# Optimization experiments

Hardware: AMD Instinct MI355X
Metric: run time of the kernel (lower is better)

The kernel has to match this reference:

```python
import jax, jax.numpy as jnp
import numpy as np

EMB = 1024
HEAD = 128

def setup_inputs() -> dict:
    key = jax.random.key(0)
    kx, kk, kq, kv = jax.random.split(key, 4)
    s = 1.0 / np.sqrt(EMB)
    return {
        "x": jax.random.normal(kx, (8, 2048, EMB), dtype=jnp.float32),
        "Wk": jax.random.normal(kk, (EMB, HEAD), dtype=jnp.float32) * s,
        "Wq": jax.random.normal(kq, (EMB, HEAD), dtype=jnp.float32) * s,
        "Wv": jax.random.normal(kv, (EMB, HEAD), dtype=jnp.float32) * s,
    }

def reference(x, Wk, Wq, Wv):
    # x: [B,T,E]; projections (no bias)
    k = jnp.einsum('bte,eh->bth', x, Wk)
    q = jnp.einsum('bte,eh->bth', x, Wq)
    v = jnp.einsum('bte,eh->bth', x, Wv)
    # scores: [B,T,T], NOTE: no 1/sqrt(d) scaling in original module
    qk = jnp.einsum('bih,bjh->bij', q, k)
    T = x.shape[1]
    causal = jnp.tril(jnp.ones((T, T), dtype=bool))  # True = keep
    qk = jnp.where(causal, qk, -jnp.inf)
    # NOTE: softmax over axis -2 (query axis), as in original
    attn = jax.nn.softmax(qk, axis=-2)
    return jnp.einsum('bij,bjh->bih', attn, v)
```

## Files before the change

kernel.cpp:

```cpp
#include <hip/hip_runtime.h>

typedef unsigned short u16;
typedef unsigned int u32;
typedef _Float16 f16;
typedef __attribute__((ext_vector_type(8))) _Float16 f16x8;
typedef __attribute__((ext_vector_type(4))) float f32x4;

constexpr int SEQ = 2048;
constexpr int EMBD = 1024;
constexpr int HD = 128;
constexpr int NB = 8;
constexpr int NSLS = 8;
constexpr int NSLP = 4;

__device__ inline u16 f2h(float f) { return __builtin_bit_cast(u16, (f16)f); }
__device__ inline u32 pack2(float a, float b) { return (u32)f2h(a) | ((u32)f2h(b) << 16); }

__device__ inline f32x4 mfma16(f16x8 a, f16x8 b, f32x4 c) {
  return __builtin_amdgcn_mfma_f32_16x16x32_f16(a, b, c, 0, 0, 0);
}

__device__ __forceinline__ void gload16(const u16* g, u16* l) {
  __builtin_amdgcn_global_load_lds(
      (const __attribute__((address_space(1))) u32*)g,
      (__attribute__((address_space(3))) u32*)l, 16, 0, 0);
}

template<int RB>
__device__ inline f16x8 frag_ld(const u16* lds, int row, int e) {
  int byte = row * RB + ((e * 2) ^ ((row & 7) << 4));
  return *reinterpret_cast<const f16x8*>(reinterpret_cast<const char*>(lds) + byte);
}

__global__ __launch_bounds__(256) void k_cvt_w(const float* __restrict__ Wq,
                                               const float* __restrict__ Wk,
                                               const float* __restrict__ Wv,
                                               u16* __restrict__ Wt) {
  int t = blockIdx.x * 256 + threadIdx.x;
  int e0 = (t & 255) * 4;
  int H = t >> 8;
  int w = H >> 7, h = H & 127;
  const float* W = (w == 0) ? Wq : (w == 1) ? Wk : Wv;
  ushort4 o;
  o.x = f2h(W[(size_t)(e0 + 0) * HD + h]);
  o.y = f2h(W[(size_t)(e0 + 1) * HD + h]);
  o.z = f2h(W[(size_t)(e0 + 2) * HD + h]);
  o.w = f2h(W[(size_t)(e0 + 3) * HD + h]);
  int k0t = e0 >> 6, ec = e0 & 63;
  size_t el = (size_t)(k0t * 384 + H) * 64 + (ec ^ ((H & 7) << 3));
  *reinterpret_cast<ushort4*>(Wt + el) = o;
}

__global__ __launch_bounds__(512, 4) void k_proj(const float* __restrict__ x,
                                                 const u16* __restrict__ Wt,
                                                 u16* __restrict__ Qb,
                                                 u16* __restrict__ Kb,
                                                 u16* __restrict__ Vtb) {
  __shared__ __align__(16) u16 As[2][64 * 64];
  __shared__ __align__(16) u16 Bs[2][192 * 64];
  const int mt = blockIdx.x, ny = blockIdx.y;
  const int t = threadIdx.x, lane = t & 63, wave = t >> 6;
  const int rh = (wave & 1) * 32, cq = (wave >> 1) * 48;
  const int ar = t >> 3, ac = t & 7;
  const float* asrc = x + (size_t)(mt * 64 + ar) * EMBD + ac * 8;
  const int adst = ar * 64 + ((ac * 8) ^ ((ar & 7) << 3));
  f32x4 zero = {0.f, 0.f, 0.f, 0.f};
  f32x4 acc[2][3];
#pragma unroll
  for (int a = 0; a < 2; ++a)
#pragma unroll
    for (int b = 0; b < 3; ++b) acc[a][b] = zero;

  float4 xe0, xe1, xo0, xo1;
  xe0 = *reinterpret_cast<const float4*>(asrc);
  xe1 = *reinterpret_cast<const float4*>(asrc + 4);
#pragma unroll
  for (int q = 0; q < 3; ++q) {
    int lin = q * 512 + t;
    gload16(Wt + ny * 12288 + lin * 8, &Bs[0][lin * 8]);
  }
  {
    uint4 o = {pack2(xe0.x, xe0.y), pack2(xe0.z, xe0.w), pack2(xe1.x, xe1.y), pack2(xe1.z, xe1.w)};
    *reinterpret_cast<uint4*>(&As[0][adst]) = o;
  }
  xo0 = *reinterpret_cast<const float4*>(asrc + 64);
  xo1 = *reinterpret_cast<const float4*>(asrc + 68);
  __syncthreads();
#pragma unroll 2
  for (int s = 0; s < 16; ++s) {
    const int cur = s & 1;
    if (s + 1 < 16) {
#pragma unroll
      for (int q = 0; q < 3; ++q) {
        int lin = q * 512 + t;
        gload16(Wt + (s + 1) * 24576 + ny * 12288 + lin * 8, &Bs[cur ^ 1][lin * 8]);
      }
    }
    if (s + 2 < 16) {
      if (cur == 0) {
        xe0 = *reinterpret_cast<const float4*>(asrc + (s + 2) * 64);
        xe1 = *reinterpret_cast<const float4*>(asrc + (s + 2) * 64 + 4);
      } else {
        xo0 = *reinterpret_cast<const float4*>(asrc + (s + 2) * 64);
        xo1 = *reinterpret_cast<const float4*>(asrc + (s + 2) * 64 + 4);
      }
    }
    __builtin_amdgcn_s_setprio(1);
#pragma unroll
    for (int kk = 0; kk < 2; ++kk) {
      f16x8 af0 = frag_ld<128>(As[cur], rh + (lane & 15), kk * 32 + (lane >> 4) * 8);
      f16x8 af1 = frag_ld<128>(As[cur], rh + 16 + (lane & 15), kk * 32 + (lane >> 4) * 8);
#pragma unroll
      for (int fc = 0; fc < 3; ++fc) {
        f16x8 bw = frag_ld<128>(Bs[cur], cq + fc * 16 + (lane & 15), kk * 32 + (lane >> 4) * 8);
        acc[0][fc] = mfma16(af0, bw, acc[0][fc]);
        acc[1][fc] = mfma16(af1, bw, acc[1][fc]);
      }
    }
    __builtin_amdgcn_s_setprio(0);
    if (s + 1 < 16) {
      uint4 o;
      if (cur == 0)
        o = {pack2(xo0.x, xo0.y), pack2(xo0.z, xo0.w), pack2(xo1.x, xo1.y), pack2(xo1.z, xo1.w)};
      else
        o = {pack2(xe0.x, xe0.y), pack2(xe0.z, xe0.w), pack2(xe1.x, xe1.y), pack2(xe1.z, xe1.w)};
      *reinterpret_cast<uint4*>(&As[cur ^ 1][adst]) = o;
    }
    __syncthreads();
  }
#pragma unroll
  for (int fi = 0; fi < 2; ++fi)
#pragma unroll
    for (int fc = 0; fc < 3; ++fc) {
      int gcol = ny * 192 + cq + fc * 16 + (lane & 15);
      int w = gcol >> 7, h = gcol & 127;
      int i0 = mt * 64 + rh + fi * 16 + (lane >> 4) * 4;
      if (w < 2) {
        u16* P = w ? Kb : Qb;
#pragma unroll
        for (int r = 0; r < 4; ++r) {
          int i = i0 + r;
          P[(size_t)i * 128 + (h ^ ((i & 7) << 3))] = f2h(acc[fi][fc][r]);
        }
      } else {
        int bb = i0 >> 11, jt = (i0 >> 6) & 31, tl = i0 & 63;
        ushort4 o = {f2h(acc[fi][fc][0]), f2h(acc[fi][fc][1]),
                     f2h(acc[fi][fc][2]), f2h(acc[fi][fc][3])};
        size_t el = ((size_t)(bb * 32 + jt) * 128 + h) * 64 + (tl ^ ((h & 7) << 3));
        *reinterpret_cast<ushort4*>(Vtb + el) = o;
      }
    }
}

__device__ inline void merge_ml(float& m, float& l, float m2, float l2) {
  float mn = fmaxf(m, m2);
  float a = (m > -1e37f) ? l * __expf(m - mn) : 0.f;
  float b = (m2 > -1e37f) ? l2 * __expf(m2 - mn) : 0.f;
  m = mn;
  l = a + b;
}

__global__ __launch_bounds__(256, 2) void k_statsA(const u16* __restrict__ Qb,
                                                   const u16* __restrict__ Kb,
                                                   float* __restrict__ mpart,
                                                   float* __restrict__ lpart) {
  __shared__ __align__(16) u16 Qs[2][128 * 128];
  const int id = blockIdx.y * 64 + blockIdx.x;
  const int bb = id & 7, z = (id >> 3) & 7, sl = id >> 6;
  const int t = threadIdx.x, lane = t & 63, wj = (t >> 6) * 32;
  f32x4 zero = {0.f, 0.f, 0.f, 0.f};

  for (int ph = 0; ph < 2; ++ph) {
    const int jt = ph ? 15 - z : z;
    __syncthreads();
#pragma unroll
    for (int q = 0; q < 8; ++q) {
      int lin = q * 256 + t;
      gload16(Kb + ((size_t)bb * SEQ + jt * 128) * 128 + lin * 8, &Qs[0][lin * 8]);
    }
    __syncthreads();
    f16x8 af[2][4];
#pragma unroll
    for (int fj = 0; fj < 2; ++fj)
#pragma unroll
      for (int kk = 0; kk < 4; ++kk)
        af[fj][kk] = frag_ld<256>(Qs[0], wj + fj * 16 + (lane & 15), kk * 32 + (lane >> 4) * 8);
    float m[2][4], l[2][4];
#pragma unroll
    for (int a = 0; a < 2; ++a)
#pragma unroll
      for (int r = 0; r < 4; ++r) {
        m[a][r] = -INFINITY;
        l[a][r] = 0.f;
      }
    const int it0 = jt + ((sl - jt) & 7);
    int cur = 1;
    if (it0 < 16) {
#pragma unroll
      for (int q = 0; q < 8; ++q) {
        int lin = q * 256 + t;
        gload16(Qb + ((size_t)bb * SEQ + it0 * 128) * 128 + lin * 8, &Qs[1][lin * 8]);
      }
      for (int it = it0; it < 16; it += 8) {
        __syncthreads();
        if (it + 8 < 16) {
#pragma unroll
          for (int q = 0; q < 8; ++q) {
            int lin = q * 256 + t;
            gload16(Qb + ((size_t)bb * SEQ + (it + 8) * 128) * 128 + lin * 8,
                    &Qs[cur ^ 1][lin * 8]);
          }
        }
        f32x4 acc[2][8];
#pragma unroll
        for (int a = 0; a < 2; ++a)
#pragma unroll
          for (int b = 0; b < 8; ++b) acc[a][b] = zero;
        __builtin_amdgcn_s_setprio(1);
#pragma unroll
        for (int kk = 0; kk < 4; ++kk)
#pragma unroll
          for (int fi = 0; fi < 8; ++fi) {
            f16x8 bq = frag_ld<256>(Qs[cur], fi * 16 + (lane & 15), kk * 32 + (lane >> 4) * 8);
            acc[0][fi] = mfma16(af[0][kk], bq, acc[0][fi]);
            acc[1][fi] = mfma16(af[1][kk], bq, acc[1][fi]);
          }
        __builtin_amdgcn_s_setprio(0);
        if (it == jt) {
#pragma unroll
          for (int fj = 0; fj < 2; ++fj)
#pragma unroll
            for (int r = 0; r < 4; ++r) {
              int jg = jt * 128 + wj + fj * 16 + (lane >> 4) * 4 + r;
              float v[8];
              float vmax = -INFINITY;
#pragma unroll
              for (int fi = 0; fi < 8; ++fi) {
                int ig = it * 128 + fi * 16 + (lane & 15);
                v[fi] = (ig >= jg) ? acc[fj][fi][r] : -INFINITY;
                vmax = fmaxf(vmax, v[fi]);
              }
              if (vmax > -1e37f) {
                float mn = fmaxf(m[fj][r], vmax);
                float sc = (m[fj][r] > -1e37f) ? __expf(m[fj][r] - mn) : 0.f;
                float ss = 0.f;
#pragma unroll
                for (int fi = 0; fi < 8; ++fi)
                  ss += (v[fi] > -1e37f) ? __expf(v[fi] - mn) : 0.f;
                l[fj][r] = l[fj][r] * sc + ss;
                m[fj][r] = mn;
              }
            }
        } else {
#pragma unroll
          for (int fj = 0; fj < 2; ++fj)
#pragma unroll
            for (int r = 0; r < 4; ++r) {
              float vmax = acc[fj][0][r];
#pragma unroll
              for (int fi = 1; fi < 8; ++fi) vmax = fmaxf(vmax, acc[fj][fi][r]);
              float mn = fmaxf(m[fj][r], vmax);
              float sc = __expf(m[fj][r] - mn);
              float ss = 0.f;
#pragma unroll
              for (int fi = 0; fi < 8; ++fi) ss += __expf(acc[fj][fi][r] - mn);
              l[fj][r] = l[fj][r] * sc + ss;
              m[fj][r] = mn;
            }
        }
        cur ^= 1;
      }
    }
#pragma unroll
    for (int fj = 0; fj < 2; ++fj)
#pragma unroll
      for (int r = 0; r < 4; ++r)
        for (int msk = 1; msk <= 8; msk <<= 1) {
          float m2 = __shfl_xor(m[fj][r], msk);
          float l2 = __shfl_xor(l[fj][r], msk);
          merge_ml(m[fj][r], l[fj][r], m2, l2);
        }
    if ((lane & 15) == 0) {
#pragma unroll
      for (int fj = 0; fj < 2; ++fj)
#pragma unroll
        for (int r = 0; r < 4; ++r) {
          int j = jt * 128 + wj + fj * 16 + (lane >> 4) * 4 + r;
          size_t idx = (size_t)sl * (NB * SEQ) + (size_t)bb * SEQ + j;
          mpart[idx] = m[fj][r];
          lpart[idx] = l[fj][r];
        }
    }
  }
}

__global__ __launch_bounds__(256) void k_stats_reduce(const float* __restrict__ mpart,
                                                      const float* __restrict__ lpart,
                                                      float* __restrict__ Cg) {
  int idx = blockIdx.x * 256 + threadIdx.x;
  float m = -INFINITY;
#pragma unroll
  for (int sl = 0; sl < NSLS; sl++) m = fmaxf(m, mpart[sl * (NB * SEQ) + idx]);
  float l = 0.f;
#pragma unroll
  for (int sl = 0; sl < NSLS; sl++) {
    float ms = mpart[sl * (NB * SEQ) + idx];
    if (ms > -1e37f) l += lpart[sl * (NB * SEQ) + idx] * __expf(ms - m);
  }
  Cg[idx] = m + __logf(l);
}

__global__ __launch_bounds__(256, 2) void k_passB(const u16* __restrict__ Qb,
                                                  const u16* __restrict__ Kb,
                                                  const u16* __restrict__ Vtb,
                                                  const float* __restrict__ Cg,
                                                  u16* __restrict__ opart) {
  __shared__ __align__(16) u16 Ks2[2][64 * 128];
  __shared__ __align__(16) u16 Vs2[2][128 * 64];
  __shared__ __align__(16) u16 Ps[64 * 64];
  const int id = blockIdx.y * 64 + blockIdx.x;
  const int bb = id & 7, zp = (id >> 3) & 15, sl = id >> 7;
  const int t = threadIdx.x, lane = t & 63, wave = t >> 6;
  f32x4 zero = {0.f, 0.f, 0.f, 0.f};

  auto stageKV = [&](int jt, int b) {
#pragma unroll
    for (int q = 0; q < 4; ++q) {
      int lin = q * 256 + t;
      gload16(Kb + ((size_t)bb * SEQ + jt * 64) * 128 + lin * 8, &Ks2[b][lin * 8]);
    }
#pragma unroll
    for (int q = 0; q < 4; ++q) {
      int lin = q * 256 + t;
      gload16(Vtb + ((size_t)bb * 32 + jt) * 8192 + lin * 8, &Vs2[b][lin * 8]);
    }
  };

  for (int ph = 0; ph < 2; ++ph) {
    const int it = ph ? 31 - zp : zp;
    f16x8 qf[4];
#pragma unroll
    for (int kk = 0; kk < 4; ++kk) {
      size_t gi = (size_t)bb * SEQ + it * 64 + wave * 16 + (lane & 15);
      int e0 = kk * 32 + (lane >> 4) * 8;
      qf[kk] = *reinterpret_cast<const f16x8*>(Qb + gi * 128 + (e0 ^ (((int)gi & 7) << 3)));
    }
    f32x4 accO[8];
#pragma unroll
    for (int b = 0; b < 8; ++b) accO[b] = zero;
    __syncthreads();
    if (sl <= it) stageKV(sl, 0);
    int cur = 0;
    for (int jt = sl; jt <= it; jt += NSLP) {
      __syncthreads();
      if (jt + NSLP <= it) stageKV(jt + NSLP, cur ^ 1);
      float cj[4];
#pragma unroll
      for (int fj = 0; fj < 4; ++fj)
        cj[fj] = Cg[bb * SEQ + jt * 64 + fj * 16 + (lane & 15)];
      f32x4 accS[4];
#pragma unroll
      for (int b = 0; b < 4; ++b) accS[b] = zero;
      __builtin_amdgcn_s_setprio(1);
#pragma unroll
      for (int kk = 0; kk < 4; ++kk)
#pragma unroll
        for (int fj = 0; fj < 4; ++fj) {
          f16x8 bk = frag_ld<256>(Ks2[cur], fj * 16 + (lane & 15), kk * 32 + (lane >> 4) * 8);
          accS[fj] = mfma16(qf[kk], bk, accS[fj]);
        }
      __builtin_amdgcn_s_setprio(0);
#pragma unroll
      for (int fj = 0; fj < 4; ++fj) {
        int jloc = fj * 16 + (lane & 15);
        int jg = jt * 64 + jloc;
        float c = cj[fj];
#pragma unroll
        for (int r = 0; r < 4; ++r) {
          int iloc = wave * 16 + (lane >> 4) * 4 + r;
          int ig = it * 64 + iloc;
          float p = __expf(accS[fj][r] - c);
          if (ig < jg) p = 0.f;
          Ps[iloc * 64 + (jloc ^ ((iloc & 7) << 3))] = f2h(p);
        }
      }
      __builtin_amdgcn_s_setprio(1);
#pragma unroll
      for (int ks = 0; ks < 2; ++ks) {
        f16x8 pa = frag_ld<128>(Ps, wave * 16 + (lane & 15), ks * 32 + (lane >> 4) * 8);
#pragma unroll
        for (int fh = 0; fh < 8; ++fh) {
          f16x8 bv = frag_ld<128>(Vs2[cur], fh * 16 + (lane & 15), ks * 32 + (lane >> 4) * 8);
          accO[fh] = mfma16(pa, bv, accO[fh]);
        }
      }
      __builtin_amdgcn_s_setprio(0);
      cur ^= 1;
    }
#pragma unroll
    for (int fh = 0; fh < 8; ++fh)
#pragma unroll
      for (int r = 0; r < 4; ++r) {
        int ig = it * 64 + wave * 16 + (lane >> 4) * 4 + r;
        int h = fh * 16 + (lane & 15);
        opart[(((size_t)sl * NB + bb) * SEQ + ig) * HD + h] = f2h(accO[fh][r]);
      }
  }
}

__global__ __launch_bounds__(256) void k_reduceB(const u16* __restrict__ opart,
                                                 float* __restrict__ out) {
  size_t base = ((size_t)blockIdx.x * 256 + threadIdx.x) * 8;
  const size_t S = (size_t)NB * SEQ * HD;
  float s[8];
#pragma unroll
  for (int j = 0; j < 8; j++) s[j] = 0.f;
#pragma unroll
  for (int sl = 0; sl < NSLP; sl++) {
    f16x8 v = *reinterpret_cast<const f16x8*>(opart + sl * S + base);
#pragma unroll
    for (int j = 0; j < 8; j++) s[j] += (float)v[j];
  }
  float4 o0 = {s[0], s[1], s[2], s[3]};
  float4 o1 = {s[4], s[5], s[6], s[7]};
  *reinterpret_cast<float4*>(out + base) = o0;
  *reinterpret_cast<float4*>(out + base + 4) = o1;
}

extern "C" void kernel_launch(void* const* d_in, const int* in_sizes, int n_in,
                              void* d_out, int out_size, void* d_ws, size_t ws_size,
                              hipStream_t stream) {
  (void)in_sizes; (void)n_in; (void)out_size; (void)ws_size;
  const float* x = (const float*)d_in[0];
  const float* Wk = (const float*)d_in[1];
  const float* Wq = (const float*)d_in[2];
  const float* Wv = (const float*)d_in[3];
  float* out = (float*)d_out;
  char* ws = (char*)d_ws;

  u16* Wt = (u16*)(ws + 0);
  u16* Qb = (u16*)(ws + 786432);
  u16* Kb = (u16*)(ws + 4980736);
  u16* Vtb = (u16*)(ws + 9175040);
  float* mpart = (float*)(ws + 13369344);
  float* lpart = (float*)(ws + 13893632);
  float* Cg = (float*)(ws + 14417920);
  u16* opart = (u16*)(ws + 14483456);

  k_cvt_w<<<384, 256, 0, stream>>>(Wq, Wk, Wv, Wt);
  k_proj<<<dim3(256, 2), 512, 0, stream>>>(x, Wt, Qb, Kb, Vtb);
  k_statsA<<<dim3(64, 8), 256, 0, stream>>>(Qb, Kb, mpart, lpart);
  k_stats_reduce<<<64, 256, 0, stream>>>(mpart, lpart, Cg);
  k_passB<<<dim3(64, 8), 256, 0, stream>>>(Qb, Kb, Vtb, Cg, opart);
  k_reduceB<<<1024, 256, 0, stream>>>(opart, out);
}
```

Baseline: 79.15 us.

## Widen projection and passB tiles to reuse loaded operands across more rows

The projection kernel now computes all 384 output columns per block, so each x tile is loaded and converted once instead of twice, at the cost of double the LDS for weights and lower occupancy. PassB switches to 128-row query tiles with each wave handling two 16-row fragments, reusing every staged K/V tile for twice as many queries. To keep the grid size, the key dimension is split into 8 slices instead of 4. This doubles the partial-output buffer that k_reduceB sums, and the workspace offsets are shifted to fit.

```diff
diff --git a/kernel.cpp b/kernel.cpp
--- a/kernel.cpp
+++ b/kernel.cpp
@@ -11,7 +11,7 @@
 constexpr int HD = 128;
 constexpr int NB = 8;
 constexpr int NSLS = 8;
-constexpr int NSLP = 4;
+constexpr int NSLP = 8;
 
 __device__ inline u16 f2h(float f) { return __builtin_bit_cast(u16, (f16)f); }
 __device__ inline u32 pack2(float a, float b) { return (u32)f2h(a) | ((u32)f2h(b) << 16); }
@@ -51,33 +51,33 @@
   *reinterpret_cast<ushort4*>(Wt + el) = o;
 }
 
-__global__ __launch_bounds__(512, 4) void k_proj(const float* __restrict__ x,
+__global__ __launch_bounds__(512, 2) void k_proj(const float* __restrict__ x,
                                                  const u16* __restrict__ Wt,
                                                  u16* __restrict__ Qb,
                                                  u16* __restrict__ Kb,
                                                  u16* __restrict__ Vtb) {
   __shared__ __align__(16) u16 As[2][64 * 64];
-  __shared__ __align__(16) u16 Bs[2][192 * 64];
-  const int mt = blockIdx.x, ny = blockIdx.y;
+  __shared__ __align__(16) u16 Bs[2][384 * 64];
+  const int mt = blockIdx.x;
   const int t = threadIdx.x, lane = t & 63, wave = t >> 6;
-  const int rh = (wave & 1) * 32, cq = (wave >> 1) * 48;
+  const int rh = (wave & 1) * 32, cq = (wave >> 1) * 96;
   const int ar = t >> 3, ac = t & 7;
   const float* asrc = x + (size_t)(mt * 64 + ar) * EMBD + ac * 8;
   const int adst = ar * 64 + ((ac * 8) ^ ((ar & 7) << 3));
   f32x4 zero = {0.f, 0.f, 0.f, 0.f};
-  f32x4 acc[2][3];
+  f32x4 acc[2][6];
 #pragma unroll
   for (int a = 0; a < 2; ++a)
 #pragma unroll
-    for (int b = 0; b < 3; ++b) acc[a][b] = zero;
+    for (int b = 0; b < 6; ++b) acc[a][b] = zero;
 
   float4 xe0, xe1, xo0, xo1;
   xe0 = *reinterpret_cast<const float4*>(asrc);
   xe1 = *reinterpret_cast<const float4*>(asrc + 4);
 #pragma unroll
-  for (int q = 0; q < 3; ++q) {
+  for (int q = 0; q < 6; ++q) {
     int lin = q * 512 + t;
-    gload16(Wt + ny * 12288 + lin * 8, &Bs[0][lin * 8]);
+    gload16(Wt + lin * 8, &Bs[0][lin * 8]);
   }
   {
     uint4 o = {pack2(xe0.x, xe0.y), pack2(xe0.z, xe0.w), pack2(xe1.x, xe1.y), pack2(xe1.z, xe1.w)};
@@ -91,9 +91,9 @@
     const int cur = s & 1;
     if (s + 1 < 16) {
 #pragma unroll
-      for (int q = 0; q < 3; ++q) {
+      for (int q = 0; q < 6; ++q) {
         int lin = q * 512 + t;
-        gload16(Wt + (s + 1) * 24576 + ny * 12288 + lin * 8, &Bs[cur ^ 1][lin * 8]);
+        gload16(Wt + (s + 1) * 24576 + lin * 8, &Bs[cur ^ 1][lin * 8]);
       }
     }
     if (s + 2 < 16) {
@@ -111,7 +111,7 @@
       f16x8 af0 = frag_ld<128>(As[cur], rh + (lane & 15), kk * 32 + (lane >> 4) * 8);
       f16x8 af1 = frag_ld<128>(As[cur], rh + 16 + (lane & 15), kk * 32 + (lane >> 4) * 8);
 #pragma unroll
-      for (int fc = 0; fc < 3; ++fc) {
+      for (int fc = 0; fc < 6; ++fc) {
         f16x8 bw = frag_ld<128>(Bs[cur], cq + fc * 16 + (lane & 15), kk * 32 + (lane >> 4) * 8);
         acc[0][fc] = mfma16(af0, bw, acc[0][fc]);
         acc[1][fc] = mfma16(af1, bw, acc[1][fc]);
@@ -131,8 +131,8 @@
 #pragma unroll
   for (int fi = 0; fi < 2; ++fi)
 #pragma unroll
-    for (int fc = 0; fc < 3; ++fc) {
-      int gcol = ny * 192 + cq + fc * 16 + (lane & 15);
+    for (int fc = 0; fc < 6; ++fc) {
+      int gcol = cq + fc * 16 + (lane & 15);
       int w = gcol >> 7, h = gcol & 127;
       int i0 = mt * 64 + rh + fi * 16 + (lane >> 4) * 4;
       if (w < 2) {
@@ -165,7 +165,7 @@
                                                    float* __restrict__ mpart,
                                                    float* __restrict__ lpart) {
   __shared__ __align__(16) u16 Qs[2][128 * 128];
-  const int id = blockIdx.y * 64 + blockIdx.x;
+  const int id = blockIdx.x;
   const int bb = id & 7, z = (id >> 3) & 7, sl = id >> 6;
   const int t = threadIdx.x, lane = t & 63, wj = (t >> 6) * 32;
   f32x4 zero = {0.f, 0.f, 0.f, 0.f};
@@ -317,10 +317,10 @@
                                                   u16* __restrict__ opart) {
   __shared__ __align__(16) u16 Ks2[2][64 * 128];
   __shared__ __align__(16) u16 Vs2[2][128 * 64];
-  __shared__ __align__(16) u16 Ps[64 * 64];
-  const int id = blockIdx.y * 64 + blockIdx.x;
-  const int bb = id & 7, zp = (id >> 3) & 15, sl = id >> 7;
-  const int t = threadIdx.x, lane = t & 63, wave = t >> 6;
+  __shared__ __align__(16) u16 Ps[128 * 64];
+  const int id = blockIdx.x;
+  const int bb = id & 7, z = (id >> 3) & 7, sl = id >> 6;
+  const int t = threadIdx.x, lane = t & 63, wi = (t >> 6) * 32;
   f32x4 zero = {0.f, 0.f, 0.f, 0.f};
 
   auto stageKV = [&](int jt, int b) {
@@ -337,37 +337,45 @@
   };
 
   for (int ph = 0; ph < 2; ++ph) {
-    const int it = ph ? 31 - zp : zp;
-    f16x8 qf[4];
-#pragma unroll
-    for (int kk = 0; kk < 4; ++kk) {
-      size_t gi = (size_t)bb * SEQ + it * 64 + wave * 16 + (lane & 15);
-      int e0 = kk * 32 + (lane >> 4) * 8;
-      qf[kk] = *reinterpret_cast<const f16x8*>(Qb + gi * 128 + (e0 ^ (((int)gi & 7) << 3)));
-    }
-    f32x4 accO[8];
-#pragma unroll
-    for (int b = 0; b < 8; ++b) accO[b] = zero;
+    const int it = ph ? 15 - z : z;
+    f16x8 qf[2][4];
+#pragma unroll
+    for (int fi = 0; fi < 2; ++fi)
+#pragma unroll
+      for (int kk = 0; kk < 4; ++kk) {
+        size_t gi = (size_t)bb * SEQ + it * 128 + wi + fi * 16 + (lane & 15);
+        int e0 = kk * 32 + (lane >> 4) * 8;
+        qf[fi][kk] = *reinterpret_cast<const f16x8*>(Qb + gi * 128 + (e0 ^ (((int)gi & 7) << 3)));
+      }
+    f32x4 accO[2][8];
+#pragma unroll
+    for (int a = 0; a < 2; ++a)
+#pragma unroll
+      for (int b = 0; b < 8; ++b) accO[a][b] = zero;
+    const int jtmax = 2 * it + 1;
     __syncthreads();
-    if (sl <= it) stageKV(sl, 0);
+    if (sl <= jtmax) stageKV(sl, 0);
     int cur = 0;
-    for (int jt = sl; jt <= it; jt += NSLP) {
+    for (int jt = sl; jt <= jtmax; jt += NSLP) {
       __syncthreads();
-      if (jt + NSLP <= it) stageKV(jt + NSLP, cur ^ 1);
+      if (jt + NSLP <= jtmax) stageKV(jt + NSLP, cur ^ 1);
       float cj[4];
 #pragma unroll
       for (int fj = 0; fj < 4; ++fj)
         cj[fj] = Cg[bb * SEQ + jt * 64 + fj * 16 + (lane & 15)];
-      f32x4 accS[4];
-#pragma unroll
-      for (int b = 0; b < 4; ++b) accS[b] = zero;
+      f32x4 accS[2][4];
+#pragma unroll
+      for (int a = 0; a < 2; ++a)
+#pragma unroll
+        for (int b = 0; b < 4; ++b) accS[a][b] = zero;
       __builtin_amdgcn_s_setprio(1);
 #pragma unroll
       for (int kk = 0; kk < 4; ++kk)
 #pragma unroll
         for (int fj = 0; fj < 4; ++fj) {
           f16x8 bk = frag_ld<256>(Ks2[cur], fj * 16 + (lane & 15), kk * 32 + (lane >> 4) * 8);
-          accS[fj] = mfma16(qf[kk], bk, accS[fj]);
+          accS[0][fj] = mfma16(qf[0][kk], bk, accS[0][fj]);
+          accS[1][fj] = mfma16(qf[1][kk], bk, accS[1][fj]);
         }
       __builtin_amdgcn_s_setprio(0);
 #pragma unroll
@@ -376,35 +384,41 @@
         int jg = jt * 64 + jloc;
         float c = cj[fj];
 #pragma unroll
-        for (int r = 0; r < 4; ++r) {
-          int iloc = wave * 16 + (lane >> 4) * 4 + r;
-          int ig = it * 64 + iloc;
-          float p = __expf(accS[fj][r] - c);
-          if (ig < jg) p = 0.f;
-          Ps[iloc * 64 + (jloc ^ ((iloc & 7) << 3))] = f2h(p);
-        }
+        for (int fi = 0; fi < 2; ++fi)
+#pragma unroll
+          for (int r = 0; r < 4; ++r) {
+            int iloc = wi + fi * 16 + (lane >> 4) * 4 + r;
+            int ig = it * 128 + iloc;
+            float p = __expf(accS[fi][fj][r] - c);
+            if (ig < jg) p = 0.f;
+            Ps[iloc * 64 + (jloc ^ ((iloc & 7) << 3))] = f2h(p);
+          }
       }
       __builtin_amdgcn_s_setprio(1);
 #pragma unroll
       for (int ks = 0; ks < 2; ++ks) {
-        f16x8 pa = frag_ld<128>(Ps, wave * 16 + (lane & 15), ks * 32 + (lane >> 4) * 8);
+        f16x8 pa0 = frag_ld<128>(Ps, wi + (lane & 15), ks * 32 + (lane >> 4) * 8);
+        f16x8 pa1 = frag_ld<128>(Ps, wi + 16 + (lane & 15), ks * 32 + (lane >> 4) * 8);
 #pragma unroll
         for (int fh = 0; fh < 8; ++fh) {
           f16x8 bv = frag_ld<128>(Vs2[cur], fh * 16 + (lane & 15), ks * 32 + (lane >> 4) * 8);
-          accO[fh] = mfma16(pa, bv, accO[fh]);
+          accO[0][fh] = mfma16(pa0, bv, accO[0][fh]);
+          accO[1][fh] = mfma16(pa1, bv, accO[1][fh]);
         }
       }
       __builtin_amdgcn_s_setprio(0);
       cur ^= 1;
     }
 #pragma unroll
-    for (int fh = 0; fh < 8; ++fh)
-#pragma unroll
-      for (int r = 0; r < 4; ++r) {
-        int ig = it * 64 + wave * 16 + (lane >> 4) * 4 + r;
-        int h = fh * 16 + (lane & 15);
-        opart[(((size_t)sl * NB + bb) * SEQ + ig) * HD + h] = f2h(accO[fh][r]);
-      }
+    for (int fi = 0; fi < 2; ++fi)
+#pragma unroll
+      for (int fh = 0; fh < 8; ++fh)
+#pragma unroll
+        for (int r = 0; r < 4; ++r) {
+          int ig = it * 128 + wi + fi * 16 + (lane >> 4) * 4 + r;
+          int h = fh * 16 + (lane & 15);
+          opart[(((size_t)sl * NB + bb) * SEQ + ig) * HD + h] = f2h(accO[fi][fh][r]);
+        }
   }
 }
 
@@ -445,12 +459,12 @@
   float* mpart = (float*)(ws + 13369344);
   float* lpart = (float*)(ws + 13893632);
   float* Cg = (float*)(ws + 14417920);
-  u16* opart = (u16*)(ws + 14483456);
+  u16* opart = (u16*)(ws + 14548992);
 
   k_cvt_w<<<384, 256, 0, stream>>>(Wq, Wk, Wv, Wt);
-  k_proj<<<dim3(256, 2), 512, 0, stream>>>(x, Wt, Qb, Kb, Vtb);
-  k_statsA<<<dim3(64, 8), 256, 0, stream>>>(Qb, Kb, mpart, lpart);
+  k_proj<<<256, 512, 0, stream>>>(x, Wt, Qb, Kb, Vtb);
+  k_statsA<<<512, 256, 0, stream>>>(Qb, Kb, mpart, lpart);
   k_stats_reduce<<<64, 256, 0, stream>>>(mpart, lpart, Cg);
-  k_passB<<<dim3(64, 8), 256, 0, stream>>>(Qb, Kb, Vtb, Cg, opart);
+  k_passB<<<512, 256, 0, stream>>>(Qb, Kb, Vtb, Cg, opart);
   k_reduceB<<<1024, 256, 0, stream>>>(opart, out);
 }
```

New measurement: 84.06 us. 1.06x slower.

## Enlarge statsA key tile to 256 rows per block for more register reuse

Applied to the files above, without the earlier changes.

The stats kernel now gives each block 256 key rows instead of 128, with 64 rows per wave held as four A-fragment sets, and loads the key tile into both LDS buffers. Each query tile is processed in two halves of 64 columns, so every B fragment feeds four MFMAs instead of two. This raises MFMA work per LDS read and halves how often query tiles are re-staged per key row. The cost is more registers per wave and an extra barrier before the query buffer is reused. Grids become 1-D and the opart workspace offset is moved.

```diff
diff --git a/kernel.cpp b/kernel.cpp
--- a/kernel.cpp
+++ b/kernel.cpp
@@ -165,41 +165,45 @@
                                                    float* __restrict__ mpart,
                                                    float* __restrict__ lpart) {
   __shared__ __align__(16) u16 Qs[2][128 * 128];
-  const int id = blockIdx.y * 64 + blockIdx.x;
-  const int bb = id & 7, z = (id >> 3) & 7, sl = id >> 6;
-  const int t = threadIdx.x, lane = t & 63, wj = (t >> 6) * 32;
+  const int id = blockIdx.x;
+  const int bb = id & 7, zp = (id >> 3) & 7, sl = id >> 6;
+  const int t = threadIdx.x, lane = t & 63, wave = t >> 6;
   f32x4 zero = {0.f, 0.f, 0.f, 0.f};
 
   for (int ph = 0; ph < 2; ++ph) {
-    const int jt = ph ? 15 - z : z;
+    const int jb = ph ? 7 - zp : zp;
     __syncthreads();
 #pragma unroll
-    for (int q = 0; q < 8; ++q) {
+    for (int q = 0; q < 16; ++q) {
       int lin = q * 256 + t;
-      gload16(Kb + ((size_t)bb * SEQ + jt * 128) * 128 + lin * 8, &Qs[0][lin * 8]);
+      gload16(Kb + ((size_t)bb * SEQ + jb * 256) * 128 + lin * 8, &Qs[0][lin * 8]);
     }
     __syncthreads();
-    f16x8 af[2][4];
-#pragma unroll
-    for (int fj = 0; fj < 2; ++fj)
-#pragma unroll
-      for (int kk = 0; kk < 4; ++kk)
-        af[fj][kk] = frag_ld<256>(Qs[0], wj + fj * 16 + (lane & 15), kk * 32 + (lane >> 4) * 8);
-    float m[2][4], l[2][4];
-#pragma unroll
-    for (int a = 0; a < 2; ++a)
+    f16x8 af[4][4];
+#pragma unroll
+    for (int fj = 0; fj < 4; ++fj)
+#pragma unroll
+      for (int kk = 0; kk < 4; ++kk) {
+        int row = wave * 64 + fj * 16 + (lane & 15);
+        af[fj][kk] = frag_ld<256>(Qs[row >> 7], row & 127, kk * 32 + (lane >> 4) * 8);
+      }
+    float m[4][4], l[4][4];
+#pragma unroll
+    for (int fj = 0; fj < 4; ++fj)
 #pragma unroll
       for (int r = 0; r < 4; ++r) {
-        m[a][r] = -INFINITY;
-        l[a][r] = 0.f;
-      }
-    const int it0 = jt + ((sl - jt) & 7);
-    int cur = 1;
+        m[fj][r] = -INFINITY;
+        l[fj][r] = 0.f;
+      }
+    __syncthreads();
+    const int itb = 2 * jb;
+    const int it0 = itb + ((sl - itb) & 7);
+    int cur = 0;
     if (it0 < 16) {
 #pragma unroll
       for (int q = 0; q < 8; ++q) {
         int lin = q * 256 + t;
-        gload16(Qb + ((size_t)bb * SEQ + it0 * 128) * 128 + lin * 8, &Qs[1][lin * 8]);
+        gload16(Qb + ((size_t)bb * SEQ + it0 * 128) * 128 + lin * 8, &Qs[0][lin * 8]);
       }
       for (int it = it0; it < 16; it += 8) {
         __syncthreads();
@@ -211,68 +215,74 @@
                     &Qs[cur ^ 1][lin * 8]);
           }
         }
-        f32x4 acc[2][8];
-#pragma unroll
-        for (int a = 0; a < 2; ++a)
-#pragma unroll
-          for (int b = 0; b < 8; ++b) acc[a][b] = zero;
-        __builtin_amdgcn_s_setprio(1);
-#pragma unroll
-        for (int kk = 0; kk < 4; ++kk)
-#pragma unroll
-          for (int fi = 0; fi < 8; ++fi) {
-            f16x8 bq = frag_ld<256>(Qs[cur], fi * 16 + (lane & 15), kk * 32 + (lane >> 4) * 8);
-            acc[0][fi] = mfma16(af[0][kk], bq, acc[0][fi]);
-            acc[1][fi] = mfma16(af[1][kk], bq, acc[1][fi]);
-          }
-        __builtin_amdgcn_s_setprio(0);
-        if (it == jt) {
-#pragma unroll
-          for (int fj = 0; fj < 2; ++fj)
-#pragma unroll
-            for (int r = 0; r < 4; ++r) {
-              int jg = jt * 128 + wj + fj * 16 + (lane >> 4) * 4 + r;
-              float v[8];
-              float vmax = -INFINITY;
-#pragma unroll
-              for (int fi = 0; fi < 8; ++fi) {
-                int ig = it * 128 + fi * 16 + (lane & 15);
-                v[fi] = (ig >= jg) ? acc[fj][fi][r] : -INFINITY;
-                vmax = fmaxf(vmax, v[fi]);
+        const bool diag = (it <= 2 * jb + 1);
+#pragma unroll
+        for (int h = 0; h < 2; ++h) {
+          f32x4 acc[4][4];
+#pragma unroll
+          for (int a = 0; a < 4; ++a)
+#pragma unroll
+            for (int b = 0; b < 4; ++b) acc[a][b] = zero;
+          __builtin_amdgcn_s_setprio(1);
+#pragma unroll
+          for (int kk = 0; kk < 4; ++kk)
+#pragma unroll
+            for (int fi = 0; fi < 4; ++fi) {
+              f16x8 bq = frag_ld<256>(Qs[cur], (h * 4 + fi) * 16 + (lane & 15),
+                                      kk * 32 + (lane >> 4) * 8);
+#pragma unroll
+              for (int fj = 0; fj < 4; ++fj)
+                acc[fj][fi] = mfma16(af[fj][kk], bq, acc[fj][fi]);
+            }
+          __builtin_amdgcn_s_setprio(0);
+          if (diag) {
+#pragma unroll
+            for (int fj = 0; fj < 4; ++fj)
+#pragma unroll
+              for (int r = 0; r < 4; ++r) {
+                int jg = jb * 256 + wave * 64 + fj * 16 + (lane >> 4) * 4 + r;
+                float v[4];
+                float vmax = -INFINITY;
+#pragma unroll
+                for (int fi = 0; fi < 4; ++fi) {
+                  int ig = it * 128 + (h * 4 + fi) * 16 + (lane & 15);
+                  v[fi] = (ig >= jg) ? acc[fj][fi][r] : -INFINITY;
+                  vmax = fmaxf(vmax, v[fi]);
+                }
+                if (vmax > -1e37f) {
+                  float mn = fmaxf(m[fj][r], vmax);
+                  float sc = (m[fj][r] > -1e37f) ? __expf(m[fj][r] - mn) : 0.f;
+                  float ss = 0.f;
+#pragma unroll
+                  for (int fi = 0; fi < 4; ++fi)
+                    ss += (v[fi] > -1e37f) ? __expf(v[fi] - mn) : 0.f;
+                  l[fj][r] = l[fj][r] * sc + ss;
+                  m[fj][r] = mn;
+                }
               }
-              if (vmax > -1e37f) {
+          } else {
+#pragma unroll
+            for (int fj = 0; fj < 4; ++fj)
+#pragma unroll
+              for (int r = 0; r < 4; ++r) {
+                float vmax = acc[fj][0][r];
+#pragma unroll
+                for (int fi = 1; fi < 4; ++fi) vmax = fmaxf(vmax, acc[fj][fi][r]);
                 float mn = fmaxf(m[fj][r], vmax);
-                float sc = (m[fj][r] > -1e37f) ? __expf(m[fj][r] - mn) : 0.f;
+                float sc = __expf(m[fj][r] - mn);
                 float ss = 0.f;
 #pragma unroll
-                for (int fi = 0; fi < 8; ++fi)
-                  ss += (v[fi] > -1e37f) ? __expf(v[fi] - mn) : 0.f;
+                for (int fi = 0; fi < 4; ++fi) ss += __expf(acc[fj][fi][r] - mn);
                 l[fj][r] = l[fj][r] * sc + ss;
                 m[fj][r] = mn;
               }
-            }
-        } else {
-#pragma unroll
-          for (int fj = 0; fj < 2; ++fj)
-#pragma unroll
-            for (int r = 0; r < 4; ++r) {
-              float vmax = acc[fj][0][r];
-#pragma unroll
-              for (int fi = 1; fi < 8; ++fi) vmax = fmaxf(vmax, acc[fj][fi][r]);
-              float mn = fmaxf(m[fj][r], vmax);
-              float sc = __expf(m[fj][r] - mn);
-              float ss = 0.f;
-#pragma unroll
-              for (int fi = 0; fi < 8; ++fi) ss += __expf(acc[fj][fi][r] - mn);
-              l[fj][r] = l[fj][r] * sc + ss;
-              m[fj][r] = mn;
-            }
+          }
         }
         cur ^= 1;
       }
     }
 #pragma unroll
-    for (int fj = 0; fj < 2; ++fj)
+    for (int fj = 0; fj < 4; ++fj)
 #pragma unroll
       for (int r = 0; r < 4; ++r)
         for (int msk = 1; msk <= 8; msk <<= 1) {
@@ -282,10 +292,10 @@
         }
     if ((lane & 15) == 0) {
 #pragma unroll
-      for (int fj = 0; fj < 2; ++fj)
+      for (int fj = 0; fj < 4; ++fj)
 #pragma unroll
         for (int r = 0; r < 4; ++r) {
-          int j = jt * 128 + wj + fj * 16 + (lane >> 4) * 4 + r;
+          int j = jb * 256 + wave * 64 + fj * 16 + (lane >> 4) * 4 + r;
           size_t idx = (size_t)sl * (NB * SEQ) + (size_t)bb * SEQ + j;
           mpart[idx] = m[fj][r];
           lpart[idx] = l[fj][r];
@@ -318,7 +328,7 @@
   __shared__ __align__(16) u16 Ks2[2][64 * 128];
   __shared__ __align__(16) u16 Vs2[2][128 * 64];
   __shared__ __align__(16) u16 Ps[64 * 64];
-  const int id = blockIdx.y * 64 + blockIdx.x;
+  const int id = blockIdx.x;
   const int bb = id & 7, zp = (id >> 3) & 15, sl = id >> 7;
   const int t = threadIdx.x, lane = t & 63, wave = t >> 6;
   f32x4 zero = {0.f, 0.f, 0.f, 0.f};
@@ -445,12 +455,12 @@
   float* mpart = (float*)(ws + 13369344);
   float* lpart = (float*)(ws + 13893632);
   float* Cg = (float*)(ws + 14417920);
-  u16* opart = (u16*)(ws + 14483456);
+  u16* opart = (u16*)(ws + 14548992);
 
   k_cvt_w<<<384, 256, 0, stream>>>(Wq, Wk, Wv, Wt);
   k_proj<<<dim3(256, 2), 512, 0, stream>>>(x, Wt, Qb, Kb, Vtb);
-  k_statsA<<<dim3(64, 8), 256, 0, stream>>>(Qb, Kb, mpart, lpart);
+  k_statsA<<<512, 256, 0, stream>>>(Qb, Kb, mpart, lpart);
   k_stats_reduce<<<64, 256, 0, stream>>>(mpart, lpart, Cg);
-  k_passB<<<dim3(64, 8), 256, 0, stream>>>(Qb, Kb, Vtb, Cg, opart);
+  k_passB<<<512, 256, 0, stream>>>(Qb, Kb, Vtb, Cg, opart);
   k_reduceB<<<1024, 256, 0, stream>>>(opart, out);
 }
```

New measurement: 94.52 us. +19.4%, slower.

## Use 32x32 MFMA with 128-row query tiles and eight KV slices in passB

Applied to the files above, without the earlier changes.

Rewrites the attention pass to use 32x32x16 MFMA instructions, with each wave owning 32 query rows so a block covers 128 query rows instead of 64. The KV split count rises from 4 to 8 so the grid stays at 512 blocks, and the grids are flattened to 1D. The goal is fewer fragment loads per FLOP and better reuse of K and V tiles. In exchange it doubles the partial output buffer that k_reduceB must sum, and reduceB's loop over NSLP now reads eight slices.

```diff
diff --git a/kernel.cpp b/kernel.cpp
--- a/kernel.cpp
+++ b/kernel.cpp
@@ -5,19 +5,23 @@
 typedef _Float16 f16;
 typedef __attribute__((ext_vector_type(8))) _Float16 f16x8;
 typedef __attribute__((ext_vector_type(4))) float f32x4;
+typedef __attribute__((ext_vector_type(16))) float f32x16;
 
 constexpr int SEQ = 2048;
 constexpr int EMBD = 1024;
 constexpr int HD = 128;
 constexpr int NB = 8;
 constexpr int NSLS = 8;
-constexpr int NSLP = 4;
+constexpr int NSLP = 8;
 
 __device__ inline u16 f2h(float f) { return __builtin_bit_cast(u16, (f16)f); }
 __device__ inline u32 pack2(float a, float b) { return (u32)f2h(a) | ((u32)f2h(b) << 16); }
 
 __device__ inline f32x4 mfma16(f16x8 a, f16x8 b, f32x4 c) {
   return __builtin_amdgcn_mfma_f32_16x16x32_f16(a, b, c, 0, 0, 0);
+}
+__device__ inline f32x16 mfma32(f16x8 a, f16x8 b, f32x16 c) {
+  return __builtin_amdgcn_mfma_f32_32x32x16_f16(a, b, c, 0, 0, 0);
 }
 
 __device__ __forceinline__ void gload16(const u16* g, u16* l) {
@@ -165,7 +169,7 @@
                                                    float* __restrict__ mpart,
                                                    float* __restrict__ lpart) {
   __shared__ __align__(16) u16 Qs[2][128 * 128];
-  const int id = blockIdx.y * 64 + blockIdx.x;
+  const int id = blockIdx.x;
   const int bb = id & 7, z = (id >> 3) & 7, sl = id >> 6;
   const int t = threadIdx.x, lane = t & 63, wj = (t >> 6) * 32;
   f32x4 zero = {0.f, 0.f, 0.f, 0.f};
@@ -317,11 +321,11 @@
                                                   u16* __restrict__ opart) {
   __shared__ __align__(16) u16 Ks2[2][64 * 128];
   __shared__ __align__(16) u16 Vs2[2][128 * 64];
-  __shared__ __align__(16) u16 Ps[64 * 64];
-  const int id = blockIdx.y * 64 + blockIdx.x;
-  const int bb = id & 7, zp = (id >> 3) & 15, sl = id >> 7;
+  __shared__ __align__(16) u16 Ps[128 * 64];
+  const int id = blockIdx.x;
+  const int bb = id & 7, z = (id >> 3) & 7, sl = id >> 6;
   const int t = threadIdx.x, lane = t & 63, wave = t >> 6;
-  f32x4 zero = {0.f, 0.f, 0.f, 0.f};
+  const int l31 = lane & 31, lh = lane >> 5;
 
   auto stageKV = [&](int jt, int b) {
 #pragma unroll
@@ -337,74 +341,84 @@
   };
 
   for (int ph = 0; ph < 2; ++ph) {
-    const int it = ph ? 31 - zp : zp;
-    f16x8 qf[4];
-#pragma unroll
-    for (int kk = 0; kk < 4; ++kk) {
-      size_t gi = (size_t)bb * SEQ + it * 64 + wave * 16 + (lane & 15);
-      int e0 = kk * 32 + (lane >> 4) * 8;
-      qf[kk] = *reinterpret_cast<const f16x8*>(Qb + gi * 128 + (e0 ^ (((int)gi & 7) << 3)));
-    }
-    f32x4 accO[8];
-#pragma unroll
-    for (int b = 0; b < 8; ++b) accO[b] = zero;
+    const int it = ph ? 15 - z : z;
+    f16x8 qa[8];
+    {
+      size_t gi = (size_t)bb * SEQ + it * 128 + wave * 32 + l31;
+      const u16* qrow = Qb + gi * 128;
+      int sw = ((int)gi & 7) << 3;
+#pragma unroll
+      for (int ks = 0; ks < 8; ++ks) {
+        int e0 = ks * 16 + lh * 8;
+        qa[ks] = *reinterpret_cast<const f16x8*>(qrow + (e0 ^ sw));
+      }
+    }
+    f32x16 accO[4];
+#pragma unroll
+    for (int b = 0; b < 4; ++b)
+#pragma unroll
+      for (int q = 0; q < 16; ++q) accO[b][q] = 0.f;
+    const int jtmax = 2 * it + 1;
     __syncthreads();
-    if (sl <= it) stageKV(sl, 0);
+    if (sl <= jtmax) stageKV(sl, 0);
     int cur = 0;
-    for (int jt = sl; jt <= it; jt += NSLP) {
+    for (int jt = sl; jt <= jtmax; jt += NSLP) {
       __syncthreads();
-      if (jt + NSLP <= it) stageKV(jt + NSLP, cur ^ 1);
-      float cj[4];
-#pragma unroll
-      for (int fj = 0; fj < 4; ++fj)
-        cj[fj] = Cg[bb * SEQ + jt * 64 + fj * 16 + (lane & 15)];
-      f32x4 accS[4];
-#pragma unroll
-      for (int b = 0; b < 4; ++b) accS[b] = zero;
+      if (jt + NSLP <= jtmax) stageKV(jt + NSLP, cur ^ 1);
+      float cj[2];
+#pragma unroll
+      for (int jtile = 0; jtile < 2; ++jtile)
+        cj[jtile] = Cg[bb * SEQ + jt * 64 + jtile * 32 + l31];
+      f32x16 accS[2];
+#pragma unroll
+      for (int b = 0; b < 2; ++b)
+#pragma unroll
+        for (int q = 0; q < 16; ++q) accS[b][q] = 0.f;
       __builtin_amdgcn_s_setprio(1);
 #pragma unroll
-      for (int kk = 0; kk < 4; ++kk)
-#pragma unroll
-        for (int fj = 0; fj < 4; ++fj) {
-          f16x8 bk = frag_ld<256>(Ks2[cur], fj * 16 + (lane & 15), kk * 32 + (lane >> 4) * 8);
-          accS[fj] = mfma16(qf[kk], bk, accS[fj]);
+      for (int ks = 0; ks < 8; ++ks)
+#pragma unroll
+        for (int jtile = 0; jtile < 2; ++jtile) {
+          f16x8 bk = frag_ld<256>(Ks2[cur], jtile * 32 + l31, ks * 16 + lh * 8);
+          accS[jtile] = mfma32(qa[ks], bk, accS[jtile]);
         }
       __builtin_amdgcn_s_setprio(0);
 #pragma unroll
-      for (int fj = 0; fj < 4; ++fj) {
-        int jloc = fj * 16 + (lane & 15);
+      for (int jtile = 0; jtile < 2; ++jtile) {
+        int jloc = jtile * 32 + l31;
         int jg = jt * 64 + jloc;
-        float c = cj[fj];
-#pragma unroll
-        for (int r = 0; r < 4; ++r) {
-          int iloc = wave * 16 + (lane >> 4) * 4 + r;
-          int ig = it * 64 + iloc;
-          float p = __expf(accS[fj][r] - c);
+        float c = cj[jtile];
+#pragma unroll
+        for (int q = 0; q < 16; ++q) {
+          int iloc = wave * 32 + (q & 3) + 8 * (q >> 2) + 4 * lh;
+          int ig = it * 128 + iloc;
+          float p = __expf(accS[jtile][q] - c);
           if (ig < jg) p = 0.f;
           Ps[iloc * 64 + (jloc ^ ((iloc & 7) << 3))] = f2h(p);
         }
       }
       __builtin_amdgcn_s_setprio(1);
 #pragma unroll
-      for (int ks = 0; ks < 2; ++ks) {
-        f16x8 pa = frag_ld<128>(Ps, wave * 16 + (lane & 15), ks * 32 + (lane >> 4) * 8);
-#pragma unroll
-        for (int fh = 0; fh < 8; ++fh) {
-          f16x8 bv = frag_ld<128>(Vs2[cur], fh * 16 + (lane & 15), ks * 32 + (lane >> 4) * 8);
-          accO[fh] = mfma16(pa, bv, accO[fh]);
+      for (int js = 0; js < 4; ++js) {
+        f16x8 pa = frag_ld<128>(Ps, wave * 32 + l31, js * 16 + lh * 8);
+#pragma unroll
+        for (int sh = 0; sh < 4; ++sh) {
+          f16x8 bv = frag_ld<128>(Vs2[cur], sh * 32 + l31, js * 16 + lh * 8);
+          accO[sh] = mfma32(pa, bv, accO[sh]);
         }
       }
       __builtin_amdgcn_s_setprio(0);
       cur ^= 1;
     }
 #pragma unroll
-    for (int fh = 0; fh < 8; ++fh)
-#pragma unroll
-      for (int r = 0; r < 4; ++r) {
-        int ig = it * 64 + wave * 16 + (lane >> 4) * 4 + r;
-        int h = fh * 16 + (lane & 15);
-        opart[(((size_t)sl * NB + bb) * SEQ + ig) * HD + h] = f2h(accO[fh][r]);
-      }
+    for (int sh = 0; sh < 4; ++sh) {
+      int h = sh * 32 + l31;
+#pragma unroll
+      for (int q = 0; q < 16; ++q) {
+        int ig = it * 128 + wave * 32 + (q & 3) + 8 * (q >> 2) + 4 * lh;
+        opart[(((size_t)sl * NB + bb) * SEQ + ig) * HD + h] = f2h(accO[sh][q]);
+      }
+    }
   }
 }
 
@@ -445,12 +459,12 @@
   float* mpart = (float*)(ws + 13369344);
   float* lpart = (float*)(ws + 13893632);
   float* Cg = (float*)(ws + 14417920);
-  u16* opart = (u16*)(ws + 14483456);
+  u16* opart = (u16*)(ws + 14548992);
 
   k_cvt_w<<<384, 256, 0, stream>>>(Wq, Wk, Wv, Wt);
   k_proj<<<dim3(256, 2), 512, 0, stream>>>(x, Wt, Qb, Kb, Vtb);
-  k_statsA<<<dim3(64, 8), 256, 0, stream>>>(Qb, Kb, mpart, lpart);
+  k_statsA<<<512, 256, 0, stream>>>(Qb, Kb, mpart, lpart);
   k_stats_reduce<<<64, 256, 0, stream>>>(mpart, lpart, Cg);
-  k_passB<<<dim3(64, 8), 256, 0, stream>>>(Qb, Kb, Vtb, Cg, opart);
+  k_passB<<<512, 256, 0, stream>>>(Qb, Kb, Vtb, Cg, opart);
   k_reduceB<<<1024, 256, 0, stream>>>(opart, out);
 }
```

Measured after the change: 80.77 us. +2.0%, slower.
